# Kernel tuning notes

Hardware: AMD Instinct MI355X
Metric: run time of the kernel (lower is better)

## Reference

```python
import jax, jax.numpy as jnp
import numpy as np

B, S, D, H, HD = 2, 2048, 2048, 16, 128


def precompute_freqs_cis(dim, end, theta=10000.0):
    freqs = 1.0 / theta ** (np.arange(0, dim, 2, dtype=np.float32)[: dim // 2] / dim)
    t = np.arange(end, dtype=np.float32)
    freqs = np.outer(t, freqs)
    freqs = np.concatenate((freqs, freqs), axis=-1)  # [S, HD]
    return jnp.asarray(np.cos(freqs)), jnp.asarray(np.sin(freqs))


def rotate_half(x):
    x1, x2 = x[..., : x.shape[-1] // 2], x[..., x.shape[-1] // 2 :]
    return jnp.concatenate((-x2, x1), axis=-1)


def setup_inputs() -> dict:
    key = jax.random.key(0)
    ks = jax.random.split(key, 5)
    scale = 1.0 / np.sqrt(D)
    return {
        "x": jax.random.normal(ks[0], (B, S, D), jnp.float32),
        "mask": jnp.ones((1, 1, S, S), jnp.bool_),
        "Wq": jax.random.normal(ks[1], (D, H, HD), jnp.float32) * scale,
        "Wk": jax.random.normal(ks[2], (D, H, HD), jnp.float32) * scale,
        "Wv": jax.random.normal(ks[3], (D, H, HD), jnp.float32) * scale,
        "Wo": jax.random.normal(ks[4], (H, HD, D), jnp.float32) * scale,
    }


def reference(x, mask, Wq, Wk, Wv, Wo):
    seq_len = x.shape[1]
    head_dim = Wq.shape[-1]
    # QKV projections: [B,S,D] x [D,H,HD] -> [B,S,H,HD]
    q = jnp.einsum("bsd,dhk->bshk", x, Wq)
    k = jnp.einsum("bsd,dhk->bshk", x, Wk)
    v = jnp.einsum("bsd,dhk->bshk", x, Wv)
    # Rotary position embedding
    cos, sin = precompute_freqs_cis(head_dim, seq_len)
    cos = cos[None, :, None, :]  # [1,S,1,HD]
    sin = sin[None, :, None, :]
    q = q * cos + rotate_half(q) * sin
    k = k * cos + rotate_half(k) * sin
    # Scaled dot-product attention (flax dot_product_attention semantics)
    scores = jnp.einsum("bqhk,bskh->bhqs", q / jnp.sqrt(jnp.float32(head_dim)), k.swapaxes(-1, -2))
    big_neg = jnp.finfo(scores.dtype).min
    scores = jnp.where(mask, scores, big_neg)
    attn = jax.nn.softmax(scores, axis=-1)  # [B,H,S,S]
    ctx = jnp.einsum("bhqs,bshk->bqhk", attn, v)  # [B,S,H,HD]
    # Output projection over (head, head_dim)
    return jnp.einsum("bqhk,hkd->bqd", ctx, Wo)
```

## Files before the change

kernel.cpp:

```cpp
#include <hip/hip_runtime.h>
#include <math.h>

#define Bc   2
#define Sc   2048
#define Dc   2048
#define Hc   16
#define HDc  128
#define BSc  4096
#define HHDc 2048

typedef __bf16 bf16_t;
typedef __bf16 bf16x8 __attribute__((ext_vector_type(8)));
typedef __bf16 bf16x4 __attribute__((ext_vector_type(4)));
typedef float  f32x4  __attribute__((ext_vector_type(4)));

#define AS1(p) ((const __attribute__((address_space(1))) void*)(p))
#define AS3(p) ((__attribute__((address_space(3))) void*)(p))

#define MFMA16(a,b,c) __builtin_amdgcn_mfma_f32_16x16x32_bf16((a),(b),(c),0,0,0)

__global__ void convert_x(const float* __restrict__ x, bf16_t* __restrict__ xb)
{
    const size_t i = ((size_t)blockIdx.x * 256 + threadIdx.x) * 4;
    float4 v = *(const float4*)&x[i];
    bf16x4 o; o[0]=(bf16_t)v.x; o[1]=(bf16_t)v.y; o[2]=(bf16_t)v.z; o[3]=(bf16_t)v.w;
    *(bf16x4*)&xb[i] = o;
}

__global__ __launch_bounds__(256) void transpose_w(const float* __restrict__ in,
                                                   bf16_t* __restrict__ out)
{
    __shared__ float T[64][65];
    const int t = threadIdx.x;
    const int r0 = blockIdx.y * 64, c0 = blockIdx.x * 64;
    #pragma unroll
    for (int i = 0; i < 4; ++i) {
        int row = i * 16 + (t >> 4);
        int c4  = (t & 15) * 4;
        float4 v = *(const float4*)&in[(size_t)(r0 + row) * 2048 + c0 + c4];
        T[row][c4] = v.x; T[row][c4+1] = v.y; T[row][c4+2] = v.z; T[row][c4+3] = v.w;
    }
    __syncthreads();
    #pragma unroll
    for (int i = 0; i < 4; ++i) {
        int orow = i * 16 + (t >> 4);
        int c4   = (t & 15) * 4;
        bf16x4 o;
        #pragma unroll
        for (int j = 0; j < 4; ++j) o[j] = (bf16_t)T[c4 + j][orow];
        *(bf16x4*)&out[(size_t)(c0 + orow) * 2048 + r0 + c4] = o;
    }
}

__global__ void rope_tab(float* __restrict__ tab)
{
    const int i = blockIdx.x * 256 + threadIdx.x;
    const int j = i & 63, s = i >> 6;
    const float freq = expf(-(float)j * 0.14391156514261520f);
    float sn, cs;
    sincosf((float)s * freq, &sn, &cs);
    float2 v; v.x = cs; v.y = sn;
    *(float2*)&tab[i * 2] = v;
}

__global__ __launch_bounds__(256) void qkv_gemm(const bf16_t* __restrict__ A,
                                                const bf16_t* __restrict__ Bt,
                                                float* __restrict__ Qf,
                                                float* __restrict__ Kf,
                                                bf16_t* __restrict__ Vt)
{
    __shared__ bf16_t As[128 * 64];
    __shared__ bf16_t Bs[128 * 64];
    const int t = threadIdx.x;
    const int w = t >> 6, l = t & 63;
    const int wm = w >> 1, wn = w & 1;
    const int lane15 = l & 15, quad = l >> 4;
    const int swr = (lane15 & 7) * 8;
    const int m0 = blockIdx.y * 128, n0 = blockIdx.x * 128;

    f32x4 acc[4][4];
    #pragma unroll
    for (int i = 0; i < 4; ++i)
        #pragma unroll
        for (int j = 0; j < 4; ++j)
            #pragma unroll
            for (int c = 0; c < 4; ++c) acc[i][j][c] = 0.f;

    const int srow = w * 8 + (l >> 3);
    const int gk   = ((l & 7) * 8) ^ ((srow & 7) * 8);

    for (int k0 = 0; k0 < 2048; k0 += 64) {
        __syncthreads();
        #pragma unroll
        for (int p = 0; p < 4; ++p) {
            __builtin_amdgcn_global_load_lds(
                AS1(A + (size_t)(m0 + p * 32 + srow) * 2048 + k0 + gk),
                AS3(&As[(p * 32 + w * 8) * 64]), 16, 0, 0);
            __builtin_amdgcn_global_load_lds(
                AS1(Bt + (size_t)(n0 + p * 32 + srow) * 2048 + k0 + gk),
                AS3(&Bs[(p * 32 + w * 8) * 64]), 16, 0, 0);
        }
        __syncthreads();
        #pragma unroll
        for (int ks = 0; ks < 2; ++ks) {
            const int rc = ((ks * 4 + quad) * 8) ^ swr;
            bf16x8 a[4], b[4];
            #pragma unroll
            for (int mt = 0; mt < 4; ++mt)
                a[mt] = *(const bf16x8*)&As[(wm * 64 + mt * 16 + lane15) * 64 + rc];
            #pragma unroll
            for (int nt = 0; nt < 4; ++nt)
                b[nt] = *(const bf16x8*)&Bs[(wn * 64 + nt * 16 + lane15) * 64 + rc];
            #pragma unroll
            for (int mt = 0; mt < 4; ++mt)
                #pragma unroll
                for (int nt = 0; nt < 4; ++nt)
                    acc[mt][nt] = MFMA16(a[mt], b[nt], acc[mt][nt]);
        }
    }

    if (n0 < 4096) {
        float* __restrict__ dst = (n0 < 2048) ? Qf : Kf;
        const int nb = n0 & 2047;
        #pragma unroll
        for (int mt = 0; mt < 4; ++mt)
            #pragma unroll
            for (int nt = 0; nt < 4; ++nt)
                #pragma unroll
                for (int r = 0; r < 4; ++r) {
                    const int gm = m0 + wm * 64 + mt * 16 + quad * 4 + r;
                    const int gn = nb + wn * 64 + nt * 16 + lane15;
                    dst[(size_t)gm * 2048 + gn] = acc[mt][nt][r];
                }
    } else {
        const int nb = n0 - 4096;
        #pragma unroll
        for (int mt = 0; mt < 4; ++mt) {
            const int gm = m0 + wm * 64 + mt * 16 + quad * 4;
            const int bq = gm >> 11;
            const int s  = gm & 2047;
            #pragma unroll
            for (int nt = 0; nt < 4; ++nt) {
                const int gn = nb + wn * 64 + nt * 16 + lane15;
                const int h  = gn >> 7, hd = gn & 127;
                bf16x4 o;
                #pragma unroll
                for (int r = 0; r < 4; ++r) o[r] = (bf16_t)acc[mt][nt][r];
                *(bf16x4*)&Vt[((size_t)((bq * Hc + h) * HDc + hd)) * Sc + s] = o;
            }
        }
    }
}

__global__ __launch_bounds__(256) void gemm_bt(const bf16_t* __restrict__ A,
                                               const bf16_t* __restrict__ Bt,
                                               float* __restrict__ C)
{
    __shared__ bf16_t As[128 * 64];
    __shared__ bf16_t Bs[128 * 64];
    const int t = threadIdx.x;
    const int w = t >> 6, l = t & 63;
    const int wm = w >> 1, wn = w & 1;
    const int lane15 = l & 15, quad = l >> 4;
    const int swr = (lane15 & 7) * 8;
    const int m0 = blockIdx.y * 128, n0 = blockIdx.x * 128;

    f32x4 acc[4][4];
    #pragma unroll
    for (int i = 0; i < 4; ++i)
        #pragma unroll
        for (int j = 0; j < 4; ++j)
            #pragma unroll
            for (int c = 0; c < 4; ++c) acc[i][j][c] = 0.f;

    const int srow = w * 8 + (l >> 3);
    const int gk   = ((l & 7) * 8) ^ ((srow & 7) * 8);

    for (int k0 = 0; k0 < 2048; k0 += 64) {
        __syncthreads();
        #pragma unroll
        for (int p = 0; p < 4; ++p) {
            __builtin_amdgcn_global_load_lds(
                AS1(A + (size_t)(m0 + p * 32 + srow) * 2048 + k0 + gk),
                AS3(&As[(p * 32 + w * 8) * 64]), 16, 0, 0);
            __builtin_amdgcn_global_load_lds(
                AS1(Bt + (size_t)(n0 + p * 32 + srow) * 2048 + k0 + gk),
                AS3(&Bs[(p * 32 + w * 8) * 64]), 16, 0, 0);
        }
        __syncthreads();
        #pragma unroll
        for (int ks = 0; ks < 2; ++ks) {
            const int rc = ((ks * 4 + quad) * 8) ^ swr;
            bf16x8 a[4], b[4];
            #pragma unroll
            for (int mt = 0; mt < 4; ++mt)
                a[mt] = *(const bf16x8*)&As[(wm * 64 + mt * 16 + lane15) * 64 + rc];
            #pragma unroll
            for (int nt = 0; nt < 4; ++nt)
                b[nt] = *(const bf16x8*)&Bs[(wn * 64 + nt * 16 + lane15) * 64 + rc];
            #pragma unroll
            for (int mt = 0; mt < 4; ++mt)
                #pragma unroll
                for (int nt = 0; nt < 4; ++nt)
                    acc[mt][nt] = MFMA16(a[mt], b[nt], acc[mt][nt]);
        }
    }

    #pragma unroll
    for (int mt = 0; mt < 4; ++mt)
        #pragma unroll
        for (int nt = 0; nt < 4; ++nt)
            #pragma unroll
            for (int r = 0; r < 4; ++r) {
                const int gm = m0 + wm * 64 + mt * 16 + quad * 4 + r;
                const int gn = n0 + wn * 64 + nt * 16 + lane15;
                C[(size_t)gm * 2048 + gn] = acc[mt][nt][r];
            }
}

__global__ void rope_scale_cast(const float* __restrict__ Qf,
                                const float* __restrict__ Kf,
                                const float* __restrict__ tab,
                                bf16_t* __restrict__ Qh,
                                bf16_t* __restrict__ Kh)
{
    const int idx  = blockIdx.x * 256 + threadIdx.x;
    const int j4   = (idx & 15) * 4;
    const int h    = (idx >> 4) & (Hc - 1);
    const int sabs = idx >> 8;
    const int s    = sabs & (Sc - 1);
    const float QS = 0.08838834764831845f;

    const size_t base = (size_t)sabs * HHDc + (size_t)h * HDc + j4;
    float4 q1 = *(const float4*)&Qf[base];
    float4 q2 = *(const float4*)&Qf[base + 64];
    float4 k1 = *(const float4*)&Kf[base];
    float4 k2 = *(const float4*)&Kf[base + 64];
    float4 t0 = *(const float4*)&tab[(s * 64 + j4) * 2];
    float4 t1 = *(const float4*)&tab[(s * 64 + j4 + 2) * 2];

    bf16x4 qo1, qo2, ko1, ko2;
    #pragma unroll
    for (int c = 0; c < 4; ++c) {
        const float cs = (c < 2) ? ((c & 1) ? t0.z : t0.x) : ((c & 1) ? t1.z : t1.x);
        const float sn = (c < 2) ? ((c & 1) ? t0.w : t0.y) : ((c & 1) ? t1.w : t1.y);
        const float a = ((const float*)&q1)[c], bq = ((const float*)&q2)[c];
        const float x = ((const float*)&k1)[c], y  = ((const float*)&k2)[c];
        qo1[c] = (bf16_t)((a * cs - bq * sn) * QS);
        qo2[c] = (bf16_t)((bq * cs + a * sn) * QS);
        ko1[c] = (bf16_t)(x * cs - y * sn);
        ko2[c] = (bf16_t)(y * cs + x * sn);
    }
    *(bf16x4*)&Qh[base]      = qo1;
    *(bf16x4*)&Qh[base + 64] = qo2;
    *(bf16x4*)&Kh[base]      = ko1;
    *(bf16x4*)&Kh[base + 64] = ko2;
}

__global__ __launch_bounds__(512, 4) void attn_v7(const bf16_t* __restrict__ Q,
                                                  const bf16_t* __restrict__ K,
                                                  const bf16_t* __restrict__ Vt,
                                                  bf16_t* __restrict__ CTX)
{
    __shared__ bf16_t Ks[64 * 128];
    __shared__ bf16_t Vts[128 * 64];
    __shared__ bf16_t Ps[128 * 72];

    const int t = threadIdx.x, w = t >> 6, l = t & 63;
    const int lane15 = l & 15, quad = l >> 4;
    const int swr = (lane15 & 7) * 8;
    const int q0 = blockIdx.x * 128;
    const int b = blockIdx.y >> 4, h = blockIdx.y & 15;
    const size_t qbase = ((size_t)(b * Sc + q0)) * HHDc + h * HDc;
    const size_t vtb   = (size_t)blockIdx.y * HDc * Sc;
    const size_t kb0   = ((size_t)(b * Sc)) * HHDc + h * HDc;

    bf16x8 qf[4];
    #pragma unroll
    for (int ks = 0; ks < 4; ++ks)
        qf[ks] = *(const bf16x8*)&Q[qbase
            + (size_t)(w * 16 + lane15) * HHDc + (ks * 4 + quad) * 8];

    float m_ = -INFINITY, l_ = 0.f;

    f32x4 O[8];
    #pragma unroll
    for (int i = 0; i < 8; ++i)
        #pragma unroll
        for (int c = 0; c < 4; ++c) O[i][c] = 0.f;

    const int krow0 = w * 4 + (l >> 4);
    const int kgc   = lane15 * 8;
    const int vrow0 = w * 8 + (l >> 3);
    const int vgc   = (l & 7) * 8;

    bf16x8 kst[2], vst[2];
    #pragma unroll
    for (int p = 0; p < 2; ++p) {
        kst[p] = *(const bf16x8*)&K[kb0 + (size_t)(p * 32 + krow0) * HHDc + kgc];
        vst[p] = *(const bf16x8*)&Vt[vtb + (size_t)(p * 64 + vrow0) * Sc + vgc];
    }

    for (int kt = 0; kt < Sc / 64; ++kt) {
        __syncthreads();
        #pragma unroll
        for (int p = 0; p < 2; ++p) {
            const int rk = p * 32 + krow0;
            *(bf16x8*)&Ks[rk * 128 + (kgc ^ ((rk & 7) * 8))] = kst[p];
        }
        #pragma unroll
        for (int p = 0; p < 2; ++p) {
            const int rv = p * 64 + vrow0;
            *(bf16x8*)&Vts[rv * 64 + (vgc ^ ((rv & 7) * 8))] = vst[p];
        }
        if (kt + 1 < Sc / 64) {
            const size_t kbn = kb0 + (size_t)(kt + 1) * 64 * HHDc;
            #pragma unroll
            for (int p = 0; p < 2; ++p) {
                kst[p] = *(const bf16x8*)&K[kbn + (size_t)(p * 32 + krow0) * HHDc + kgc];
                vst[p] = *(const bf16x8*)&Vt[vtb + (size_t)(p * 64 + vrow0) * Sc
                                             + (kt + 1) * 64 + vgc];
            }
        }
        __syncthreads();

        f32x4 sc[4];
        #pragma unroll
        for (int j = 0; j < 4; ++j)
            #pragma unroll
            for (int c = 0; c < 4; ++c) sc[j][c] = 0.f;
        __builtin_amdgcn_s_setprio(1);
        #pragma unroll
        for (int ks = 0; ks < 4; ++ks) {
            const int rc = ((ks * 4 + quad) * 8) ^ swr;
            bf16x8 bk[4];
            #pragma unroll
            for (int nt = 0; nt < 4; ++nt)
                bk[nt] = *(const bf16x8*)&Ks[(nt * 16 + lane15) * 128 + rc];
            #pragma unroll
            for (int nt = 0; nt < 4; ++nt)
                sc[nt] = MFMA16(bk[nt], qf[ks], sc[nt]);
        }
        __builtin_amdgcn_s_setprio(0);

        {
            float tm = -INFINITY;
            #pragma unroll
            for (int nt = 0; nt < 4; ++nt)
                #pragma unroll
                for (int r = 0; r < 4; ++r) tm = fmaxf(tm, sc[nt][r]);
            tm = fmaxf(tm, __shfl_xor(tm, 16));
            tm = fmaxf(tm, __shfl_xor(tm, 32));
            const float mo = m_;
            const float mn = fmaxf(mo, tm);
            const float al = __expf(mo - mn);
            m_ = mn;
            float ts = 0.f;
            const int prow = (w * 16 + lane15) * 72;
            #pragma unroll
            for (int nt = 0; nt < 4; ++nt) {
                bf16x4 pw;
                #pragma unroll
                for (int r = 0; r < 4; ++r) {
                    const float p = __expf(sc[nt][r] - mn);
                    pw[r] = (bf16_t)p;
                    ts += p;
                }
                *(bf16x4*)&Ps[prow + nt * 16 + quad * 4] = pw;
            }
            ts += __shfl_xor(ts, 16);
            ts += __shfl_xor(ts, 32);
            l_ = l_ * al + ts;

            #pragma unroll
            for (int ht = 0; ht < 8; ++ht)
                #pragma unroll
                for (int c = 0; c < 4; ++c) O[ht][c] *= al;
        }

        __builtin_amdgcn_s_setprio(1);
        #pragma unroll
        for (int ks = 0; ks < 2; ++ks) {
            const int rcp = (ks * 4 + quad) * 8;
            const int rcv = rcp ^ swr;
            bf16x8 av[8];
            #pragma unroll
            for (int ht = 0; ht < 8; ++ht)
                av[ht] = *(const bf16x8*)&Vts[(ht * 16 + lane15) * 64 + rcv];
            bf16x8 bp = *(const bf16x8*)&Ps[(w * 16 + lane15) * 72 + rcp];
            #pragma unroll
            for (int ht = 0; ht < 8; ++ht)
                O[ht] = MFMA16(av[ht], bp, O[ht]);
        }
        __builtin_amdgcn_s_setprio(0);
    }

    {
        const float linv = 1.0f / l_;
        const int s = q0 + w * 16 + lane15;
        #pragma unroll
        for (int ht = 0; ht < 8; ++ht) {
            bf16x4 o;
            #pragma unroll
            for (int c = 0; c < 4; ++c) o[c] = (bf16_t)(O[ht][c] * linv);
            *(bf16x4*)&CTX[((size_t)(b * Sc + s)) * HHDc + h * HDc + ht * 16 + quad * 4] = o;
        }
    }
}

extern "C" void kernel_launch(void* const* d_in, const int* in_sizes, int n_in,
                              void* d_out, int out_size, void* d_ws, size_t ws_size,
                              hipStream_t stream)
{
    const float* x  = (const float*)d_in[0];
    const float* Wq = (const float*)d_in[2];
    const float* Wk = (const float*)d_in[3];
    const float* Wv = (const float*)d_in[4];
    const float* Wo = (const float*)d_in[5];
    float* out = (float*)d_out;

    bf16_t* W0  = (bf16_t*)d_ws;
    bf16_t* xb  = W0;
    bf16_t* WT3 = W0 + 8388608;
    bf16_t* WoT = W0 + 20971520;
    float*  Qf  = (float*)(W0 + 25165824);
    float*  Kf  = (float*)(W0 + 41943040);
    bf16_t* Vt  = W0 + 58720256;
    bf16_t* Kh  = W0;
    bf16_t* Qh  = W0 + 8388608;
    bf16_t* CTX = W0 + 25165824;
    float*  tab = out;

    dim3 tw(32, 32);

    rope_tab<<<512, 256, 0, stream>>>(tab);
    convert_x<<<8192, 256, 0, stream>>>(x, xb);
    transpose_w<<<tw, 256, 0, stream>>>(Wq, WT3);
    transpose_w<<<tw, 256, 0, stream>>>(Wk, WT3 + 4194304);
    transpose_w<<<tw, 256, 0, stream>>>(Wv, WT3 + 8388608);
    transpose_w<<<tw, 256, 0, stream>>>(Wo, WoT);

    qkv_gemm<<<dim3(48, 32), 256, 0, stream>>>(xb, WT3, Qf, Kf, Vt);

    rope_scale_cast<<<4096, 256, 0, stream>>>(Qf, Kf, tab, Qh, Kh);

    attn_v7<<<dim3(16, 32), 512, 0, stream>>>(Qh, Kh, Vt, CTX);

    gemm_bt<<<dim3(16, 32), 256, 0, stream>>>(CTX, WoT, out);
}
```

Baseline: 426.2 us.

## Rewrite QKV GEMM as 256x256 double-buffered 8-wave pipelined kernel

Replaces the 128x128, 4-wave QKV projection GEMM with a 256x256 tile kernel using 8 waves. It double-buffers LDS and interleaves global-to-LDS staging of the next k-tile with MFMA work on the current one, split into four sub-phases with explicit vmcnt waits, barriers and s_setprio. The aim is to hide global load latency and raise arithmetic intensity per block. The cost is 128KB of LDS per block and much more register pressure, and the manual waitcnt choreography is fragile to get right.

```diff
diff --git a/kernel.cpp b/kernel.cpp
--- a/kernel.cpp
+++ b/kernel.cpp
@@ -63,92 +63,160 @@
     *(float2*)&tab[i * 2] = v;
 }
 
-__global__ __launch_bounds__(256) void qkv_gemm(const bf16_t* __restrict__ A,
-                                                const bf16_t* __restrict__ Bt,
-                                                float* __restrict__ Qf,
-                                                float* __restrict__ Kf,
-                                                bf16_t* __restrict__ Vt)
-{
-    __shared__ bf16_t As[128 * 64];
-    __shared__ bf16_t Bs[128 * 64];
+template<int MS, int NS>
+__device__ __forceinline__ void mf_quad(f32x4 (&acc)[8][4],
+                                        const bf16x8 (&a)[4][2],
+                                        const bf16x8 (&b)[2][2])
+{
+    #pragma unroll
+    for (int ks = 0; ks < 2; ++ks)
+        #pragma unroll
+        for (int mf = 0; mf < 4; ++mf)
+            #pragma unroll
+            for (int nf = 0; nf < 2; ++nf)
+                acc[MS * 4 + mf][NS * 2 + nf] =
+                    MFMA16(a[mf][ks], b[nf][ks], acc[MS * 4 + mf][NS * 2 + nf]);
+}
+
+__global__ __launch_bounds__(512, 2) void qkv_gemm8(const bf16_t* __restrict__ A,
+                                                    const bf16_t* __restrict__ Bt,
+                                                    float* __restrict__ Qf,
+                                                    float* __restrict__ Kf,
+                                                    bf16_t* __restrict__ Vt)
+{
+    __shared__ bf16_t As[2][256 * 64];
+    __shared__ bf16_t Bs[2][256 * 64];
+
     const int t = threadIdx.x;
     const int w = t >> 6, l = t & 63;
-    const int wm = w >> 1, wn = w & 1;
+    const int wm = w >> 2, wn = w & 3;
     const int lane15 = l & 15, quad = l >> 4;
     const int swr = (lane15 & 7) * 8;
-    const int m0 = blockIdx.y * 128, n0 = blockIdx.x * 128;
-
-    f32x4 acc[4][4];
-    #pragma unroll
-    for (int i = 0; i < 4; ++i)
+    const int m0 = blockIdx.y * 256, n0 = blockIdx.x * 256;
+
+    const int gk = (((l & 7) ^ ((l >> 3) & 7)) * 8);
+
+    auto stageA = [&](int buf, int h, int kt) {
+        #pragma unroll
+        for (int p = 0; p < 2; ++p) {
+            const int rb = p * 128 + h * 64 + w * 8;
+            __builtin_amdgcn_global_load_lds(
+                AS1(A + (size_t)(m0 + rb + (l >> 3)) * 2048 + kt * 64 + gk),
+                AS3(&As[buf][rb * 64]), 16, 0, 0);
+        }
+    };
+    auto stageB = [&](int buf, int h, int kt) {
+        #pragma unroll
+        for (int p = 0; p < 2; ++p) {
+            const int rb = (2 * p + (w >> 2)) * 64 + h * 32 + (w & 3) * 8;
+            __builtin_amdgcn_global_load_lds(
+                AS1(Bt + (size_t)(n0 + rb + (l >> 3)) * 2048 + kt * 64 + gk),
+                AS3(&Bs[buf][rb * 64]), 16, 0, 0);
+        }
+    };
+
+    bf16x8 a[4][2], b[2][2];
+    auto rdA = [&](int buf, int msub) {
+        #pragma unroll
+        for (int mf = 0; mf < 4; ++mf)
+            #pragma unroll
+            for (int ks = 0; ks < 2; ++ks) {
+                const int ra = wm * 128 + msub * 64 + mf * 16 + lane15;
+                a[mf][ks] = *(const bf16x8*)&As[buf][ra * 64 + (((ks * 4 + quad) * 8) ^ swr)];
+            }
+    };
+    auto rdB = [&](int buf, int nsub) {
+        #pragma unroll
+        for (int nf = 0; nf < 2; ++nf)
+            #pragma unroll
+            for (int ks = 0; ks < 2; ++ks) {
+                const int rb = wn * 64 + nsub * 32 + nf * 16 + lane15;
+                b[nf][ks] = *(const bf16x8*)&Bs[buf][rb * 64 + (((ks * 4 + quad) * 8) ^ swr)];
+            }
+    };
+
+    f32x4 acc[8][4];
+    #pragma unroll
+    for (int i = 0; i < 8; ++i)
         #pragma unroll
         for (int j = 0; j < 4; ++j)
             #pragma unroll
             for (int c = 0; c < 4; ++c) acc[i][j][c] = 0.f;
 
-    const int srow = w * 8 + (l >> 3);
-    const int gk   = ((l & 7) * 8) ^ ((srow & 7) * 8);
-
-    for (int k0 = 0; k0 < 2048; k0 += 64) {
-        __syncthreads();
-        #pragma unroll
-        for (int p = 0; p < 4; ++p) {
-            __builtin_amdgcn_global_load_lds(
-                AS1(A + (size_t)(m0 + p * 32 + srow) * 2048 + k0 + gk),
-                AS3(&As[(p * 32 + w * 8) * 64]), 16, 0, 0);
-            __builtin_amdgcn_global_load_lds(
-                AS1(Bt + (size_t)(n0 + p * 32 + srow) * 2048 + k0 + gk),
-                AS3(&Bs[(p * 32 + w * 8) * 64]), 16, 0, 0);
-        }
-        __syncthreads();
-        #pragma unroll
-        for (int ks = 0; ks < 2; ++ks) {
-            const int rc = ((ks * 4 + quad) * 8) ^ swr;
-            bf16x8 a[4], b[4];
-            #pragma unroll
-            for (int mt = 0; mt < 4; ++mt)
-                a[mt] = *(const bf16x8*)&As[(wm * 64 + mt * 16 + lane15) * 64 + rc];
-            #pragma unroll
-            for (int nt = 0; nt < 4; ++nt)
-                b[nt] = *(const bf16x8*)&Bs[(wn * 64 + nt * 16 + lane15) * 64 + rc];
-            #pragma unroll
-            for (int mt = 0; mt < 4; ++mt)
-                #pragma unroll
-                for (int nt = 0; nt < 4; ++nt)
-                    acc[mt][nt] = MFMA16(a[mt], b[nt], acc[mt][nt]);
-        }
-    }
+    stageA(0, 0, 0); stageB(0, 0, 0); stageB(0, 1, 0); stageA(0, 1, 0);
+
+    for (int kt = 0; kt < 31; ++kt) {
+        const int cur = kt & 1, nxt = cur ^ 1;
+        asm volatile("s_waitcnt vmcnt(4)" ::: "memory");
+        __builtin_amdgcn_s_barrier();
+        __builtin_amdgcn_sched_barrier(0);
+        stageA(nxt, 0, kt + 1);
+        rdA(cur, 0); rdB(cur, 0);
+        __builtin_amdgcn_s_setprio(1); mf_quad<0,0>(acc, a, b); __builtin_amdgcn_s_setprio(0);
+        asm volatile("s_waitcnt vmcnt(4)" ::: "memory");
+        __builtin_amdgcn_s_barrier();
+        __builtin_amdgcn_sched_barrier(0);
+        stageB(nxt, 0, kt + 1);
+        rdB(cur, 1);
+        __builtin_amdgcn_s_setprio(1); mf_quad<0,1>(acc, a, b); __builtin_amdgcn_s_setprio(0);
+        asm volatile("s_waitcnt vmcnt(4)" ::: "memory");
+        __builtin_amdgcn_s_barrier();
+        __builtin_amdgcn_sched_barrier(0);
+        stageB(nxt, 1, kt + 1);
+        rdA(cur, 1); rdB(cur, 0);
+        __builtin_amdgcn_s_setprio(1); mf_quad<1,0>(acc, a, b); __builtin_amdgcn_s_setprio(0);
+        __builtin_amdgcn_s_barrier();
+        stageA(nxt, 1, kt + 1);
+        rdB(cur, 1);
+        __builtin_amdgcn_s_setprio(1); mf_quad<1,1>(acc, a, b); __builtin_amdgcn_s_setprio(0);
+    }
+    asm volatile("s_waitcnt vmcnt(0)" ::: "memory");
+    __builtin_amdgcn_s_barrier();
+    __builtin_amdgcn_sched_barrier(0);
+    rdA(1, 0); rdB(1, 0); mf_quad<0,0>(acc, a, b);
+    rdB(1, 1);            mf_quad<0,1>(acc, a, b);
+    rdA(1, 1); rdB(1, 0); mf_quad<1,0>(acc, a, b);
+    rdB(1, 1);            mf_quad<1,1>(acc, a, b);
 
     if (n0 < 4096) {
         float* __restrict__ dst = (n0 < 2048) ? Qf : Kf;
         const int nb = n0 & 2047;
         #pragma unroll
-        for (int mt = 0; mt < 4; ++mt)
-            #pragma unroll
-            for (int nt = 0; nt < 4; ++nt)
+        for (int msub = 0; msub < 2; ++msub)
+            #pragma unroll
+            for (int mf = 0; mf < 4; ++mf)
                 #pragma unroll
-                for (int r = 0; r < 4; ++r) {
-                    const int gm = m0 + wm * 64 + mt * 16 + quad * 4 + r;
-                    const int gn = nb + wn * 64 + nt * 16 + lane15;
-                    dst[(size_t)gm * 2048 + gn] = acc[mt][nt][r];
-                }
+                for (int nsub = 0; nsub < 2; ++nsub)
+                    #pragma unroll
+                    for (int nf = 0; nf < 2; ++nf)
+                        #pragma unroll
+                        for (int r = 0; r < 4; ++r) {
+                            const int gm = m0 + wm * 128 + msub * 64 + mf * 16 + quad * 4 + r;
+                            const int gn = nb + wn * 64 + nsub * 32 + nf * 16 + lane15;
+                            dst[(size_t)gm * 2048 + gn] = acc[msub * 4 + mf][nsub * 2 + nf][r];
+                        }
     } else {
         const int nb = n0 - 4096;
         #pragma unroll
-        for (int mt = 0; mt < 4; ++mt) {
-            const int gm = m0 + wm * 64 + mt * 16 + quad * 4;
-            const int bq = gm >> 11;
-            const int s  = gm & 2047;
-            #pragma unroll
-            for (int nt = 0; nt < 4; ++nt) {
-                const int gn = nb + wn * 64 + nt * 16 + lane15;
-                const int h  = gn >> 7, hd = gn & 127;
-                bf16x4 o;
+        for (int msub = 0; msub < 2; ++msub)
+            #pragma unroll
+            for (int mf = 0; mf < 4; ++mf) {
+                const int gm = m0 + wm * 128 + msub * 64 + mf * 16 + quad * 4;
+                const int bq = gm >> 11;
+                const int s  = gm & 2047;
                 #pragma unroll
-                for (int r = 0; r < 4; ++r) o[r] = (bf16_t)acc[mt][nt][r];
-                *(bf16x4*)&Vt[((size_t)((bq * Hc + h) * HDc + hd)) * Sc + s] = o;
+                for (int nsub = 0; nsub < 2; ++nsub)
+                    #pragma unroll
+                    for (int nf = 0; nf < 2; ++nf) {
+                        const int gn = nb + wn * 64 + nsub * 32 + nf * 16 + lane15;
+                        const int h  = gn >> 7, hd = gn & 127;
+                        bf16x4 o;
+                        #pragma unroll
+                        for (int r = 0; r < 4; ++r)
+                            o[r] = (bf16_t)acc[msub * 4 + mf][nsub * 2 + nf][r];
+                        *(bf16x4*)&Vt[((size_t)((bq * Hc + h) * HDc + hd)) * Sc + s] = o;
+                    }
             }
-        }
     }
 }
 
@@ -440,7 +508,7 @@
     transpose_w<<<tw, 256, 0, stream>>>(Wv, WT3 + 8388608);
     transpose_w<<<tw, 256, 0, stream>>>(Wo, WoT);
 
-    qkv_gemm<<<dim3(48, 32), 256, 0, stream>>>(xb, WT3, Qf, Kf, Vt);
+    qkv_gemm8<<<dim3(24, 16), 512, 0, stream>>>(xb, WT3, Qf, Kf, Vt);
 
     rope_scale_cast<<<4096, 256, 0, stream>>>(Qf, Kf, tab, Qh, Kh);
 
```

New measurement: 469.7 us. 10.2% more time.
